# Kernel optimization log

Measured on AMD Instinct MI355X. Metric: run time of the kernel, lower is better.

Reference implementation:

```python
import jax, jax.numpy as jnp
import numpy as np

N = 50000
E = 800000
D_IN = 128
D_OUT = 128


def setup_inputs() -> dict:
    key = jax.random.key(0)
    ks = jax.random.split(key, 12)
    x = jax.random.normal(ks[0], (N, D_IN), dtype=jnp.float32)
    W1 = jax.random.normal(ks[1], (D_IN, D_OUT), dtype=jnp.float32) * (1.0 / np.sqrt(D_IN))
    b1 = jnp.zeros((D_OUT,), dtype=jnp.float32)
    W2 = jax.random.normal(ks[2], (D_IN, D_OUT), dtype=jnp.float32) * (1.0 / np.sqrt(D_IN))
    b2 = jnp.zeros((D_OUT,), dtype=jnp.float32)
    # inverted-dropout masks, p=0.5 -> values in {0, 2}
    def mask(k):
        return jnp.where(jax.random.uniform(k, (N, D_IN)) < 0.5, 0.0, 2.0).astype(jnp.float32)
    mask_pos1 = mask(ks[3])
    mask_neg1 = mask(ks[4])
    mask_pos2 = mask(ks[5])
    mask_neg2 = mask(ks[6])
    edge_index1 = jax.random.randint(ks[7], (2, E), 0, N, dtype=jnp.int32)
    edge_index2 = jax.random.randint(ks[8], (2, E), 0, N, dtype=jnp.int32)
    perm1 = jax.random.permutation(ks[9], N).astype(jnp.int32)
    perm2 = jax.random.permutation(ks[10], N).astype(jnp.int32)
    return dict(x=x, W1=W1, b1=b1, W2=W2, b2=b2,
                mask_pos1=mask_pos1, mask_neg1=mask_neg1,
                mask_pos2=mask_pos2, mask_neg2=mask_neg2,
                edge_index1=edge_index1, edge_index2=edge_index2,
                perm1=perm1, perm2=perm2)


def gcn_conv(x, W, b, edge_index):
    """PyG GCNConv: add self-loops, symmetric normalization, then x@W aggregation + bias."""
    n = x.shape[0]
    xw = x @ W  # [N, D_OUT]
    loops = jnp.arange(n, dtype=edge_index.dtype)
    src = jnp.concatenate([edge_index[0], loops])
    dst = jnp.concatenate([edge_index[1], loops])
    deg = jax.ops.segment_sum(jnp.ones_like(dst, dtype=xw.dtype), dst, num_segments=n)
    dinv = jax.lax.rsqrt(jnp.maximum(deg, 1.0))  # deg >= 1 due to self-loops
    norm = dinv[src] * dinv[dst]                 # [E+N]
    msg = xw[src] * norm[:, None]                # [E+N, D_OUT]
    out = jax.ops.segment_sum(msg, dst, num_segments=n)
    return out + b


def _branch(x, W, b, edge_index, mask_pos, mask_neg, perm):
    pos_h = jax.nn.relu(gcn_conv(x * mask_pos, W, b, edge_index))
    neg_in = (x * mask_neg)[perm]
    neg_h = jax.nn.relu(gcn_conv(neg_in, W, b, edge_index))
    summary = jnp.mean(pos_h, axis=0, keepdims=True)  # [1, D_OUT]
    return pos_h, neg_h, summary


def reference(x, W1, b1, W2, b2, mask_pos1, mask_neg1, mask_pos2, mask_neg2,
              edge_index1, edge_index2, perm1, perm2):
    p1, n1, s1 = _branch(x, W1, b1, edge_index1, mask_pos1, mask_neg1, perm1)
    p2, n2, s2 = _branch(x, W2, b2, edge_index2, mask_pos2, mask_neg2, perm2)
    return (p1, n1, s1, p2, n2, s2)
```

## Files before the change

### kernel.cpp

```cpp
#include <hip/hip_runtime.h>
#include <hip/hip_fp16.h>

#define NN 50000
#define NE 800000
#define D 128
#define GEMM_BLOCKS 3128
#define NBKT 64
#define BW 782
#define BCAP 16384

typedef _Float16 half8_t __attribute__((ext_vector_type(8)));
typedef _Float16 half4_t __attribute__((ext_vector_type(4)));
typedef float f32x4 __attribute__((ext_vector_type(4)));

__global__ void k_init(float* s1, float* s2, int* bcnt,
                       const float* __restrict__ W1, const float* __restrict__ W2,
                       _Float16* wt1, _Float16* wt2,
                       const int* __restrict__ perm1, const int* __restrict__ perm2,
                       int* pinv1, int* pinv2) {
    int i = blockIdx.x * 256 + threadIdx.x;
    if (i < NN) { pinv1[perm1[i]] = i; pinv2[perm2[i]] = i; }
    if (i < 2 * NBKT) bcnt[i] = 0;
    if (i < D) { s1[i] = 0.f; s2[i] = 0.f; }
    if (i < 16384) {
        int n = i >> 7, k = i & 127;
        wt1[n * 128 + k] = (_Float16)W1[k * 128 + n];
        wt2[n * 128 + k] = (_Float16)W2[k * 128 + n];
    }
}

__global__ void k_bucket(const int* __restrict__ src1, const int* __restrict__ dst1,
                         const int* __restrict__ src2, const int* __restrict__ dst2,
                         int* bcnt, int2* bsd1, int2* bsd2) {
    __shared__ int lcnt[128], lpos[128], gbase[128];
    int t = threadIdx.x;
    if (t < 128) { lcnt[t] = 0; lpos[t] = 0; }
    __syncthreads();

    int e0 = blockIdx.x * 256 + t;
    int s1v0=0,d1v0=0,s2v0=0,d2v0=0, s1v1=0,d1v1=0,s2v1=0,d2v1=0;
    int s1v2=0,d1v2=0,s2v2=0,d2v2=0, s1v3=0,d1v3=0,s2v3=0,d2v3=0;
    bool v0 = (e0 + 0 * 262144) < NE;
    bool v1 = (e0 + 1 * 262144) < NE;
    bool v2 = (e0 + 2 * 262144) < NE;
    bool v3 = (e0 + 3 * 262144) < NE;
    if (v0) { int e = e0;             s1v0 = src1[e]; d1v0 = dst1[e]; s2v0 = src2[e]; d2v0 = dst2[e]; }
    if (v1) { int e = e0 + 262144;    s1v1 = src1[e]; d1v1 = dst1[e]; s2v1 = src2[e]; d2v1 = dst2[e]; }
    if (v2) { int e = e0 + 2*262144;  s1v2 = src1[e]; d1v2 = dst1[e]; s2v2 = src2[e]; d2v2 = dst2[e]; }
    if (v3) { int e = e0 + 3*262144;  s1v3 = src1[e]; d1v3 = dst1[e]; s2v3 = src2[e]; d2v3 = dst2[e]; }

    if (v0) { atomicAdd(&lcnt[d1v0 / BW], 1); atomicAdd(&lcnt[NBKT + d2v0 / BW], 1); }
    if (v1) { atomicAdd(&lcnt[d1v1 / BW], 1); atomicAdd(&lcnt[NBKT + d2v1 / BW], 1); }
    if (v2) { atomicAdd(&lcnt[d1v2 / BW], 1); atomicAdd(&lcnt[NBKT + d2v2 / BW], 1); }
    if (v3) { atomicAdd(&lcnt[d1v3 / BW], 1); atomicAdd(&lcnt[NBKT + d2v3 / BW], 1); }
    __syncthreads();
    if (t < 128) gbase[t] = atomicAdd(&bcnt[t], lcnt[t]);
    __syncthreads();

    #define PLACE(sv, dv) { \
        int r = (dv) / BW; \
        int p = gbase[r] + atomicAdd(&lpos[r], 1); \
        if (p < BCAP) bsd1[r * BCAP + p] = make_int2((sv), (dv)); }
    #define PLACE2(sv, dv) { \
        int r = (dv) / BW; \
        int p = gbase[NBKT + r] + atomicAdd(&lpos[NBKT + r], 1); \
        if (p < BCAP) bsd2[r * BCAP + p] = make_int2((sv), (dv)); }
    if (v0) { PLACE(s1v0, d1v0); PLACE2(s2v0, d2v0); }
    if (v1) { PLACE(s1v1, d1v1); PLACE2(s2v1, d2v1); }
    if (v2) { PLACE(s1v2, d1v2); PLACE2(s2v2, d2v2); }
    if (v3) { PLACE(s1v3, d1v3); PLACE2(s2v3, d2v3); }
    #undef PLACE
    #undef PLACE2
}

__launch_bounds__(512)
__global__ void k_build(const int* __restrict__ bcnt,
                        const int2* __restrict__ bsd1, const int2* __restrict__ bsd2,
                        int* rp1, int* rp2, int* col1, int* col2,
                        float* dinv1, float* dinv2) {
    __shared__ int h[1024];
    __shared__ int tsum[512];
    __shared__ int tb[64];
    __shared__ int bbase;
    int t = threadIdx.x;
    int g = blockIdx.x >> 6;
    int f = blockIdx.x & 63;
    const int2* bsd = (g ? bsd2 : bsd1) + f * BCAP;
    int* rp = g ? rp2 : rp1;
    int* col = g ? col2 : col1;
    float* dinv = g ? dinv2 : dinv1;
    int n = bcnt[g * NBKT + f];
    if (n > BCAP) n = BCAP;

    h[t] = 0; h[t + 512] = 0;
    if (t < NBKT) tb[t] = bcnt[g * NBKT + t];
    __syncthreads();

    for (int i = t; i < n; i += 512) atomicAdd(&h[bsd[i].y - f * BW], 1);
    __syncthreads();
    if (t == 0) { int b = 0; for (int j = 0; j < f; j++) b += tb[j]; bbase = b; }

    int a0 = h[2 * t], a1 = h[2 * t + 1];
    int s = a0 + a1;
    tsum[t] = s;
    __syncthreads();
    for (int off = 1; off < 512; off <<= 1) {
        int add = (t >= off) ? tsum[t - off] : 0;
        __syncthreads();
        tsum[t] += add;
        __syncthreads();
    }
    int excl = tsum[t] - s + bbase;
    int idx = 2 * t, gd = f * BW + idx;
    int e0 = excl, e1 = excl + a0;
    h[2 * t] = e0; h[2 * t + 1] = e1;
    if (idx < BW && gd < NN)         { rp[gd]     = e0; dinv[gd]     = rsqrtf((float)(a0 + 1)); }
    if (idx + 1 < BW && gd + 1 < NN) { rp[gd + 1] = e1; dinv[gd + 1] = rsqrtf((float)(a1 + 1)); }
    if (f == 63 && t == 0) rp[NN] = NE;
    __syncthreads();

    for (int i = t; i < n; i += 512) {
        int2 e = bsd[i];
        int p = atomicAdd(&h[e.y - f * BW], 1);
        col[p] = e.x;
    }
}

__launch_bounds__(256)
__global__ void k_gemm(const _Float16* __restrict__ wt1, const _Float16* __restrict__ wt2,
                       const float* __restrict__ x,
                       const float* __restrict__ mp1, const float* __restrict__ mn1,
                       const float* __restrict__ mp2, const float* __restrict__ mn2,
                       const int* __restrict__ pinv1, const int* __restrict__ pinv2,
                       const float* __restrict__ dinv1, const float* __restrict__ dinv2,
                       _Float16* xwi1, _Float16* xwi2) {
    __shared__ __align__(16) _Float16 ST[4][16][136];

    int g = blockIdx.x;
    int which = g / 782;
    int bx = g - which * 782;
    const _Float16* wt = (which < 2) ? wt1 : wt2;
    const float* mask = (which == 0) ? mp1 : (which == 1) ? mn1 : (which == 2) ? mp2 : mn2;
    const int* pinv = (which == 1) ? pinv1 : (which == 3) ? pinv2 : nullptr;
    const float* dinv = (which < 2) ? dinv1 : dinv2;
    _Float16* out = ((which < 2) ? xwi1 : xwi2) + ((which & 1) ? 128 : 0);

    int t = threadIdx.x;
    int wave = t >> 6;
    int lane = t & 63;
    int quad = lane >> 4;
    int m = lane & 15;
    int tile = bx * 4 + wave;
    if (tile * 16 >= NN) return;

    int row = tile * 16 + m;
    const float* xrow = x + (long)row * D;
    const float* mrow = mask + (long)row * D;

    half8_t a[4];
    #pragma unroll
    for (int kk = 0; kk < 4; kk++) {
        int k0 = kk * 32 + quad * 8;
        f32x4 xa = *(const f32x4*)(xrow + k0);
        f32x4 xb = *(const f32x4*)(xrow + k0 + 4);
        f32x4 ma = __builtin_nontemporal_load((const f32x4*)(mrow + k0));
        f32x4 mb = __builtin_nontemporal_load((const f32x4*)(mrow + k0 + 4));
        a[kk][0] = (_Float16)(xa[0] * ma[0]);
        a[kk][1] = (_Float16)(xa[1] * ma[1]);
        a[kk][2] = (_Float16)(xa[2] * ma[2]);
        a[kk][3] = (_Float16)(xa[3] * ma[3]);
        a[kk][4] = (_Float16)(xb[0] * mb[0]);
        a[kk][5] = (_Float16)(xb[1] * mb[1]);
        a[kk][6] = (_Float16)(xb[2] * mb[2]);
        a[kk][7] = (_Float16)(xb[3] * mb[3]);
    }

    f32x4 accs[8];
    #pragma unroll
    for (int nt = 0; nt < 8; nt++) {
        const _Float16* wrow = wt + (nt * 16 + m) * 128 + quad * 8;
        f32x4 acc = {0.f, 0.f, 0.f, 0.f};
        #pragma unroll
        for (int kk = 0; kk < 4; kk++) {
            half8_t w = *(const half8_t*)(wrow + kk * 32);
            acc = __builtin_amdgcn_mfma_f32_16x16x32_f16(w, a[kk], acc, 0, 0, 0);
        }
        accs[nt] = acc;
    }

    int orow = pinv ? pinv[row] : row;
    float ds = dinv[orow];
    _Float16* st = &ST[wave][0][0];

    #pragma unroll
    for (int nt = 0; nt < 8; nt++) {
        half4_t h;
        h[0] = (_Float16)(accs[nt][0] * ds);
        h[1] = (_Float16)(accs[nt][1] * ds);
        h[2] = (_Float16)(accs[nt][2] * ds);
        h[3] = (_Float16)(accs[nt][3] * ds);
        *(half4_t*)(st + m * 136 + nt * 16 + quad * 4) = h;
    }
    #pragma unroll
    for (int p = 0; p < 4; p++) {
        int cc = (lane >> 4) + p * 4;
        half8_t v = *(const half8_t*)(st + m * 136 + cc * 8);
        *(half8_t*)(out + (long)orow * 256 + cc * 8) = v;
    }
}

__launch_bounds__(256)
__global__ void k_agg(const _Float16* __restrict__ xwi1, const _Float16* __restrict__ xwi2,
                      const int* __restrict__ rp1, const int* __restrict__ col1,
                      const float* __restrict__ dinv1,
                      const int* __restrict__ rp2, const int* __restrict__ col2,
                      const float* __restrict__ dinv2,
                      const float* __restrict__ b1, const float* __restrict__ b2,
                      float* out) {
    int g = blockIdx.y;
    const _Float16* xwi = g ? xwi2 : xwi1;
    const int* rp = g ? rp2 : rp1;
    const int* col = g ? col2 : col1;
    const float* dinv = g ? dinv2 : dinv1;
    const float* bias = g ? b2 : b1;
    float* pos_out = out + (g ? 12800128L : 0L);
    float* neg_out = out + (g ? 19200128L : 6400000L);

    int t = threadIdx.x;
    int wave = t >> 6, lane = t & 63;
    int i = blockIdx.x * 4 + wave;
    if (i >= NN) return;
    int j4 = lane * 4;

    half4_t sv = *(const half4_t*)(xwi + (long)i * 256 + j4);
    float a0 = (float)sv[0], a1 = (float)sv[1], a2 = (float)sv[2], a3 = (float)sv[3];
    int e0 = rp[i], e1 = rp[i + 1];
    int e = e0;
    for (; e + 8 <= e1; e += 8) {
        int s0 = col[e + 0], s1 = col[e + 1], s2 = col[e + 2], s3 = col[e + 3];
        int s4 = col[e + 4], s5 = col[e + 5], s6 = col[e + 6], s7 = col[e + 7];
        half4_t v0 = *(const half4_t*)(xwi + (long)s0 * 256 + j4);
        half4_t v1 = *(const half4_t*)(xwi + (long)s1 * 256 + j4);
        half4_t v2 = *(const half4_t*)(xwi + (long)s2 * 256 + j4);
        half4_t v3 = *(const half4_t*)(xwi + (long)s3 * 256 + j4);
        half4_t v4 = *(const half4_t*)(xwi + (long)s4 * 256 + j4);
        half4_t v5 = *(const half4_t*)(xwi + (long)s5 * 256 + j4);
        half4_t v6 = *(const half4_t*)(xwi + (long)s6 * 256 + j4);
        half4_t v7 = *(const half4_t*)(xwi + (long)s7 * 256 + j4);
        a0 += (float)v0[0] + (float)v1[0] + (float)v2[0] + (float)v3[0]
            + (float)v4[0] + (float)v5[0] + (float)v6[0] + (float)v7[0];
        a1 += (float)v0[1] + (float)v1[1] + (float)v2[1] + (float)v3[1]
            + (float)v4[1] + (float)v5[1] + (float)v6[1] + (float)v7[1];
        a2 += (float)v0[2] + (float)v1[2] + (float)v2[2] + (float)v3[2]
            + (float)v4[2] + (float)v5[2] + (float)v6[2] + (float)v7[2];
        a3 += (float)v0[3] + (float)v1[3] + (float)v2[3] + (float)v3[3]
            + (float)v4[3] + (float)v5[3] + (float)v6[3] + (float)v7[3];
    }
    for (; e + 4 <= e1; e += 4) {
        int s0 = col[e + 0], s1 = col[e + 1], s2 = col[e + 2], s3 = col[e + 3];
        half4_t v0 = *(const half4_t*)(xwi + (long)s0 * 256 + j4);
        half4_t v1 = *(const half4_t*)(xwi + (long)s1 * 256 + j4);
        half4_t v2 = *(const half4_t*)(xwi + (long)s2 * 256 + j4);
        half4_t v3 = *(const half4_t*)(xwi + (long)s3 * 256 + j4);
        a0 += (float)v0[0] + (float)v1[0] + (float)v2[0] + (float)v3[0];
        a1 += (float)v0[1] + (float)v1[1] + (float)v2[1] + (float)v3[1];
        a2 += (float)v0[2] + (float)v1[2] + (float)v2[2] + (float)v3[2];
        a3 += (float)v0[3] + (float)v1[3] + (float)v2[3] + (float)v3[3];
    }
    for (; e < e1; e++) {
        int s = col[e];
        half4_t v = *(const half4_t*)(xwi + (long)s * 256 + j4);
        a0 += (float)v[0]; a1 += (float)v[1]; a2 += (float)v[2]; a3 += (float)v[3];
    }
    float di = dinv[i];
    int jj = (lane < 32) ? j4 : (j4 - 128);
    const f32x4* bp = (const f32x4*)(bias + jj);
    f32x4 bv = *bp;
    f32x4 o;
    o[0] = fmaxf(0.f, di * a0 + bv[0]);
    o[1] = fmaxf(0.f, di * a1 + bv[1]);
    o[2] = fmaxf(0.f, di * a2 + bv[2]);
    o[3] = fmaxf(0.f, di * a3 + bv[3]);
    float* dst = ((lane < 32) ? pos_out : neg_out) + (long)i * D + jj;
    __builtin_nontemporal_store(o, (f32x4*)dst);
}

__launch_bounds__(256)
__global__ void k_sum(const float* __restrict__ pos1, const float* __restrict__ pos2,
                      float* s1, float* s2) {
    int g = blockIdx.y;
    const float* pos = g ? pos2 : pos1;
    float* s = g ? s2 : s1;
    int t = threadIdx.x;
    int rg = t >> 5;
    int j = (t & 31) * 4;
    float4 acc = {0.f, 0.f, 0.f, 0.f};
    for (int i = blockIdx.x * 8 + rg; i < NN; i += gridDim.x * 8) {
        float4 v = *(const float4*)(pos + (long)i * D + j);
        acc.x += v.x; acc.y += v.y; acc.z += v.z; acc.w += v.w;
    }
    __shared__ float sm[8][128];
    sm[rg][j + 0] = acc.x;
    sm[rg][j + 1] = acc.y;
    sm[rg][j + 2] = acc.z;
    sm[rg][j + 3] = acc.w;
    __syncthreads();
    if (t < 128) {
        float v = 0.f;
        for (int r = 0; r < 8; r++) v += sm[r][t];
        atomicAdd(&s[t], v * (1.0f / NN));
    }
}

extern "C" void kernel_launch(void* const* d_in, const int* in_sizes, int n_in,
                              void* d_out, int out_size, void* d_ws, size_t ws_size,
                              hipStream_t stream) {
    const float* x   = (const float*)d_in[0];
    const float* W1  = (const float*)d_in[1];
    const float* b1  = (const float*)d_in[2];
    const float* W2  = (const float*)d_in[3];
    const float* b2  = (const float*)d_in[4];
    const float* mp1 = (const float*)d_in[5];
    const float* mn1 = (const float*)d_in[6];
    const float* mp2 = (const float*)d_in[7];
    const float* mn2 = (const float*)d_in[8];
    const int* e1 = (const int*)d_in[9];
    const int* e2 = (const int*)d_in[10];
    const int* perm1 = (const int*)d_in[11];
    const int* perm2 = (const int*)d_in[12];
    const int* src1 = e1;       const int* dst1 = e1 + NE;
    const int* src2 = e2;       const int* dst2 = e2 + NE;
    float* out = (float*)d_out;

    char* w = (char*)d_ws;
    _Float16* xwi1 = (_Float16*)w; w += (size_t)NN * 256 * 2;
    _Float16* xwi2 = (_Float16*)w; w += (size_t)NN * 256 * 2;
    int* rp1 = (int*)w;   w += (size_t)(NN + 4) * 4;
    int* rp2 = (int*)w;   w += (size_t)(NN + 4) * 4;
    int* col1 = (int*)w;  w += (size_t)NE * 4;
    int* col2 = (int*)w;  w += (size_t)NE * 4;
    float* dinv1 = (float*)w; w += (size_t)NN * 4;
    float* dinv2 = (float*)w; w += (size_t)NN * 4;
    int* bcnt  = (int*)w; w += (size_t)128 * 4;
    int2* bsd1 = (int2*)w; w += (size_t)NBKT * BCAP * 8;
    int2* bsd2 = (int2*)w; w += (size_t)NBKT * BCAP * 8;
    _Float16* wt1 = (_Float16*)w; w += (size_t)D * D * 2;
    _Float16* wt2 = (_Float16*)w; w += (size_t)D * D * 2;
    int* pinv1 = (int*)w; w += (size_t)NN * 4;
    int* pinv2 = (int*)w; w += (size_t)NN * 4;

    float* s1 = out + 12800000L;
    float* s2 = out + 25600128L;
    const float* pos1 = out;
    const float* pos2 = out + 12800128L;

    k_init<<<dim3(196), 256, 0, stream>>>(s1, s2, bcnt, W1, W2, wt1, wt2,
                                          perm1, perm2, pinv1, pinv2);
    k_bucket<<<dim3(1024), 256, 0, stream>>>(src1, dst1, src2, dst2, bcnt, bsd1, bsd2);
    k_build<<<dim3(128), 512, 0, stream>>>(bcnt, bsd1, bsd2,
                                           rp1, rp2, col1, col2, dinv1, dinv2);
    k_gemm<<<dim3(GEMM_BLOCKS), 256, 0, stream>>>(wt1, wt2,
        x, mp1, mn1, mp2, mn2, pinv1, pinv2, dinv1, dinv2, xwi1, xwi2);
    k_agg<<<dim3(12500, 2), 256, 0, stream>>>(xwi1, xwi2,
                                              rp1, col1, dinv1, rp2, col2, dinv2,
                                              b1, b2, out);
    k_sum<<<dim3(128, 2), 256, 0, stream>>>(pos1, pos2, s1, s2);
}
```

Measured before the change: 457.8 us.

## Shard bucket counters into eight sub-slots to reduce global atomic contention

```diff
diff --git a/kernel.cpp b/kernel.cpp
--- a/kernel.cpp
+++ b/kernel.cpp
@@ -7,7 +7,7 @@
 #define GEMM_BLOCKS 3128
 #define NBKT 64
 #define BW 782
-#define BCAP 16384
+#define SCAP 2048
 
 typedef _Float16 half8_t __attribute__((ext_vector_type(8)));
 typedef _Float16 half4_t __attribute__((ext_vector_type(4)));
@@ -20,7 +20,7 @@
                        int* pinv1, int* pinv2) {
     int i = blockIdx.x * 256 + threadIdx.x;
     if (i < NN) { pinv1[perm1[i]] = i; pinv2[perm2[i]] = i; }
-    if (i < 2 * NBKT) bcnt[i] = 0;
+    if (i < 1024) bcnt[i] = 0;
     if (i < D) { s1[i] = 0.f; s2[i] = 0.f; }
     if (i < 16384) {
         int n = i >> 7, k = i & 127;
@@ -34,6 +34,7 @@
                          int* bcnt, int2* bsd1, int2* bsd2) {
     __shared__ int lcnt[128], lpos[128], gbase[128];
     int t = threadIdx.x;
+    int sl = blockIdx.x & 7;
     if (t < 128) { lcnt[t] = 0; lpos[t] = 0; }
     __syncthreads();
 
@@ -54,17 +55,17 @@
     if (v2) { atomicAdd(&lcnt[d1v2 / BW], 1); atomicAdd(&lcnt[NBKT + d2v2 / BW], 1); }
     if (v3) { atomicAdd(&lcnt[d1v3 / BW], 1); atomicAdd(&lcnt[NBKT + d2v3 / BW], 1); }
     __syncthreads();
-    if (t < 128) gbase[t] = atomicAdd(&bcnt[t], lcnt[t]);
+    if (t < 128) gbase[t] = atomicAdd(&bcnt[t * 8 + sl], lcnt[t]);
     __syncthreads();
 
     #define PLACE(sv, dv) { \
         int r = (dv) / BW; \
         int p = gbase[r] + atomicAdd(&lpos[r], 1); \
-        if (p < BCAP) bsd1[r * BCAP + p] = make_int2((sv), (dv)); }
+        if (p < SCAP) bsd1[(r * 8 + sl) * SCAP + p] = make_int2((sv), (dv)); }
     #define PLACE2(sv, dv) { \
         int r = (dv) / BW; \
         int p = gbase[NBKT + r] + atomicAdd(&lpos[NBKT + r], 1); \
-        if (p < BCAP) bsd2[r * BCAP + p] = make_int2((sv), (dv)); }
+        if (p < SCAP) bsd2[(r * 8 + sl) * SCAP + p] = make_int2((sv), (dv)); }
     if (v0) { PLACE(s1v0, d1v0); PLACE2(s2v0, d2v0); }
     if (v1) { PLACE(s1v1, d1v1); PLACE2(s2v1, d2v1); }
     if (v2) { PLACE(s1v2, d1v2); PLACE2(s2v2, d2v2); }
@@ -81,22 +82,35 @@
     __shared__ int h[1024];
     __shared__ int tsum[512];
     __shared__ int tb[64];
+    __shared__ int ns[8];
     __shared__ int bbase;
     int t = threadIdx.x;
     int g = blockIdx.x >> 6;
     int f = blockIdx.x & 63;
-    const int2* bsd = (g ? bsd2 : bsd1) + f * BCAP;
+    const int2* bsd = (g ? bsd2 : bsd1) + f * 8 * SCAP;
     int* rp = g ? rp2 : rp1;
     int* col = g ? col2 : col1;
     float* dinv = g ? dinv2 : dinv1;
-    int n = bcnt[g * NBKT + f];
-    if (n > BCAP) n = BCAP;
 
     h[t] = 0; h[t + 512] = 0;
-    if (t < NBKT) tb[t] = bcnt[g * NBKT + t];
-    __syncthreads();
-
-    for (int i = t; i < n; i += 512) atomicAdd(&h[bsd[i].y - f * BW], 1);
+    if (t < 8) {
+        int v = bcnt[(g * NBKT + f) * 8 + t];
+        ns[t] = (v > SCAP) ? SCAP : v;
+    }
+    if (t < NBKT) {
+        int tot = 0;
+        #pragma unroll
+        for (int s = 0; s < 8; s++) tot += bcnt[(g * NBKT + t) * 8 + s];
+        tb[t] = tot;
+    }
+    __syncthreads();
+
+    #pragma unroll
+    for (int s = 0; s < 8; s++) {
+        int n = ns[s];
+        const int2* seg = bsd + s * SCAP;
+        for (int i = t; i < n; i += 512) atomicAdd(&h[seg[i].y - f * BW], 1);
+    }
     __syncthreads();
     if (t == 0) { int b = 0; for (int j = 0; j < f; j++) b += tb[j]; bbase = b; }
 
@@ -119,10 +133,15 @@
     if (f == 63 && t == 0) rp[NN] = NE;
     __syncthreads();
 
-    for (int i = t; i < n; i += 512) {
-        int2 e = bsd[i];
-        int p = atomicAdd(&h[e.y - f * BW], 1);
-        col[p] = e.x;
+    #pragma unroll
+    for (int sg = 0; sg < 8; sg++) {
+        int n = ns[sg];
+        const int2* seg = bsd + sg * SCAP;
+        for (int i = t; i < n; i += 512) {
+            int2 e = seg[i];
+            int p = atomicAdd(&h[e.y - f * BW], 1);
+            col[p] = e.x;
+        }
     }
 }
 
@@ -294,16 +313,16 @@
     int t = threadIdx.x;
     int rg = t >> 5;
     int j = (t & 31) * 4;
-    float4 acc = {0.f, 0.f, 0.f, 0.f};
+    f32x4 acc = {0.f, 0.f, 0.f, 0.f};
     for (int i = blockIdx.x * 8 + rg; i < NN; i += gridDim.x * 8) {
-        float4 v = *(const float4*)(pos + (long)i * D + j);
-        acc.x += v.x; acc.y += v.y; acc.z += v.z; acc.w += v.w;
+        f32x4 v = __builtin_nontemporal_load((const f32x4*)(pos + (long)i * D + j));
+        acc[0] += v[0]; acc[1] += v[1]; acc[2] += v[2]; acc[3] += v[3];
     }
     __shared__ float sm[8][128];
-    sm[rg][j + 0] = acc.x;
-    sm[rg][j + 1] = acc.y;
-    sm[rg][j + 2] = acc.z;
-    sm[rg][j + 3] = acc.w;
+    sm[rg][j + 0] = acc[0];
+    sm[rg][j + 1] = acc[1];
+    sm[rg][j + 2] = acc[2];
+    sm[rg][j + 3] = acc[3];
     __syncthreads();
     if (t < 128) {
         float v = 0.f;
@@ -341,9 +360,9 @@
     int* col2 = (int*)w;  w += (size_t)NE * 4;
     float* dinv1 = (float*)w; w += (size_t)NN * 4;
     float* dinv2 = (float*)w; w += (size_t)NN * 4;
-    int* bcnt  = (int*)w; w += (size_t)128 * 4;
-    int2* bsd1 = (int2*)w; w += (size_t)NBKT * BCAP * 8;
-    int2* bsd2 = (int2*)w; w += (size_t)NBKT * BCAP * 8;
+    int* bcnt  = (int*)w; w += (size_t)1024 * 4;
+    int2* bsd1 = (int2*)w; w += (size_t)NBKT * 8 * SCAP * 8;
+    int2* bsd2 = (int2*)w; w += (size_t)NBKT * 8 * SCAP * 8;
     _Float16* wt1 = (_Float16*)w; w += (size_t)D * D * 2;
     _Float16* wt2 = (_Float16*)w; w += (size_t)D * D * 2;
     int* pinv1 = (int*)w; w += (size_t)NN * 4;
@@ -364,5 +383,5 @@
     k_agg<<<dim3(12500, 2), 256, 0, stream>>>(xwi1, xwi2,
                                               rp1, col1, dinv1, rp2, col2, dinv2,
                                               b1, b2, out);
-    k_sum<<<dim3(128, 2), 256, 0, stream>>>(pos1, pos2, s1, s2);
-}
+    k_sum<<<dim3(512, 2), 256, 0, stream>>>(pos1, pos2, s1, s2);
+}
```

After: 455.4 us. Within noise of the previous version (-0.5%).
